# Kernel tuning notes

Measured on AMD Instinct MI355X. Metric: run time of the kernel, lower is better.

## Reference

```python
import jax, jax.numpy as jnp
import numpy as np

NUM_INSTANCES = 200
H = W = 128
PIXEL_EMB = 16   # input channels to the conditional conv
CHANNELS = 8     # num_init_channels (cond-inst hidden channels)
DEPTH = 3        # parsed from network_type 'cond_inst3'
# num_params = (16*8+8) + (8*8+8) + (8*1+1) = 217
NUM_PARAMS = (PIXEL_EMB * CHANNELS + CHANNELS) + (CHANNELS * CHANNELS + CHANNELS) + (CHANNELS + 1)


def setup_inputs() -> dict:
    key = jax.random.key(0)
    k1, k2 = jax.random.split(key)
    instance_embedding = jax.random.normal(k1, (NUM_INSTANCES, NUM_PARAMS), dtype=jnp.float32)
    pixel_embedding = jax.random.normal(k2, (NUM_INSTANCES, H, W, PIXEL_EMB), dtype=jnp.float32)
    return {"instance_embedding": instance_embedding,
            "pixel_embedding": pixel_embedding,
            "training": False}


def _per_pixel_conditional_conv(x, params, channels, depth):
    """x: [N,H,W,Cin], params: [N,P]. Chained per-instance 1x1 dynamic convs."""
    in_ch = x.shape[-1]
    start = 0
    out = x
    for i in range(depth):
        ch = 1 if i == depth - 1 else channels
        n = in_ch * ch + ch
        p = params[:, start:start + n]
        start += n
        w = p[:, :in_ch * ch].reshape(-1, in_ch, ch)   # [N, Cin, Cout]
        b = p[:, in_ch * ch:]                          # [N, Cout]
        out = jnp.einsum('nhwc,nck->nhwk', out, w) + b[:, None, None, :]
        if i != depth - 1:
            out = jax.nn.relu(out)
        in_ch = ch
    return out  # [N,H,W,1]


def reference(instance_embedding, pixel_embedding, training):
    # network_type='cond_inst3': backbone and project_out are identities;
    # instance params drive a depth-3 per-pixel conditional conv.
    out = _per_pixel_conditional_conv(pixel_embedding, instance_embedding,
                                      CHANNELS, DEPTH)
    return jnp.squeeze(out, axis=-1)  # [N,H,W]
```

## Files before the change

kernel.cpp:

```cpp
#include <hip/hip_runtime.h>


constexpr int NI = 200;
constexpr int HW = 128 * 128;
constexpr int PE = 16;
constexpr int CH = 8;
constexpr int NP = PE * CH + CH + (CH * CH + CH) + (CH + 1);

constexpr int THREADS = 256;
constexpr int PPT = 4;
constexpr int PIX_PER_BLOCK = THREADS * PPT;
constexpr int BLOCKS_PER_INST = HW / PIX_PER_BLOCK;

constexpr int OFF_W0 = 0;
constexpr int OFF_B0 = 128;
constexpr int OFF_W1 = 136;
constexpr int OFF_B1 = 200;
constexpr int OFF_W2 = 208;
constexpr int OFF_B2 = 216;

__global__ __launch_bounds__(THREADS) void maskhead_kernel(
    const float* __restrict__ inst,
    const float* __restrict__ pix,
    float* __restrict__ out)
{
    __shared__ float sp[NP];
    const int n = blockIdx.x / BLOCKS_PER_INST;
    const int chunk = blockIdx.x % BLOCKS_PER_INST;
    const int t = threadIdx.x;

    if (t < NP) sp[t] = inst[n * NP + t];
    __syncthreads();

    const size_t pixBase = (size_t)n * HW + (size_t)chunk * PIX_PER_BLOCK;

    float x[PPT][PE];
#pragma unroll
    for (int p = 0; p < PPT; ++p) {
        const float4* src =
            reinterpret_cast<const float4*>(pix + (pixBase + (size_t)p * THREADS + t) * PE);
#pragma unroll
        for (int q = 0; q < 4; ++q) {
            float4 v = src[q];
            x[p][q * 4 + 0] = v.x;
            x[p][q * 4 + 1] = v.y;
            x[p][q * 4 + 2] = v.z;
            x[p][q * 4 + 3] = v.w;
        }
    }

    float a[PPT][CH];
    {
        float4 blo = *reinterpret_cast<const float4*>(&sp[OFF_B0]);
        float4 bhi = *reinterpret_cast<const float4*>(&sp[OFF_B0 + 4]);
#pragma unroll
        for (int p = 0; p < PPT; ++p) {
            a[p][0] = blo.x; a[p][1] = blo.y; a[p][2] = blo.z; a[p][3] = blo.w;
            a[p][4] = bhi.x; a[p][5] = bhi.y; a[p][6] = bhi.z; a[p][7] = bhi.w;
        }
#pragma unroll
        for (int c = 0; c < PE; ++c) {
            float4 wlo = *reinterpret_cast<const float4*>(&sp[OFF_W0 + c * CH]);
            float4 whi = *reinterpret_cast<const float4*>(&sp[OFF_W0 + c * CH + 4]);
#pragma unroll
            for (int p = 0; p < PPT; ++p) {
                const float xv = x[p][c];
                a[p][0] = fmaf(xv, wlo.x, a[p][0]);
                a[p][1] = fmaf(xv, wlo.y, a[p][1]);
                a[p][2] = fmaf(xv, wlo.z, a[p][2]);
                a[p][3] = fmaf(xv, wlo.w, a[p][3]);
                a[p][4] = fmaf(xv, whi.x, a[p][4]);
                a[p][5] = fmaf(xv, whi.y, a[p][5]);
                a[p][6] = fmaf(xv, whi.z, a[p][6]);
                a[p][7] = fmaf(xv, whi.w, a[p][7]);
            }
        }
#pragma unroll
        for (int p = 0; p < PPT; ++p)
#pragma unroll
            for (int k = 0; k < CH; ++k) a[p][k] = fmaxf(a[p][k], 0.0f);
    }

    float y[PPT][CH];
    {
        float4 blo = *reinterpret_cast<const float4*>(&sp[OFF_B1]);
        float4 bhi = *reinterpret_cast<const float4*>(&sp[OFF_B1 + 4]);
#pragma unroll
        for (int p = 0; p < PPT; ++p) {
            y[p][0] = blo.x; y[p][1] = blo.y; y[p][2] = blo.z; y[p][3] = blo.w;
            y[p][4] = bhi.x; y[p][5] = bhi.y; y[p][6] = bhi.z; y[p][7] = bhi.w;
        }
#pragma unroll
        for (int c = 0; c < CH; ++c) {
            float4 wlo = *reinterpret_cast<const float4*>(&sp[OFF_W1 + c * CH]);
            float4 whi = *reinterpret_cast<const float4*>(&sp[OFF_W1 + c * CH + 4]);
#pragma unroll
            for (int p = 0; p < PPT; ++p) {
                const float xv = a[p][c];
                y[p][0] = fmaf(xv, wlo.x, y[p][0]);
                y[p][1] = fmaf(xv, wlo.y, y[p][1]);
                y[p][2] = fmaf(xv, wlo.z, y[p][2]);
                y[p][3] = fmaf(xv, wlo.w, y[p][3]);
                y[p][4] = fmaf(xv, whi.x, y[p][4]);
                y[p][5] = fmaf(xv, whi.y, y[p][5]);
                y[p][6] = fmaf(xv, whi.z, y[p][6]);
                y[p][7] = fmaf(xv, whi.w, y[p][7]);
            }
        }
#pragma unroll
        for (int p = 0; p < PPT; ++p)
#pragma unroll
            for (int k = 0; k < CH; ++k) y[p][k] = fmaxf(y[p][k], 0.0f);
    }

    {
        float4 wlo = *reinterpret_cast<const float4*>(&sp[OFF_W2]);
        float4 whi = *reinterpret_cast<const float4*>(&sp[OFF_W2 + 4]);
        const float b2 = sp[OFF_B2];
#pragma unroll
        for (int p = 0; p < PPT; ++p) {
            float o = b2;
            o = fmaf(y[p][0], wlo.x, o);
            o = fmaf(y[p][1], wlo.y, o);
            o = fmaf(y[p][2], wlo.z, o);
            o = fmaf(y[p][3], wlo.w, o);
            o = fmaf(y[p][4], whi.x, o);
            o = fmaf(y[p][5], whi.y, o);
            o = fmaf(y[p][6], whi.z, o);
            o = fmaf(y[p][7], whi.w, o);
            out[pixBase + (size_t)p * THREADS + t] = o;
        }
    }
}

extern "C" void kernel_launch(void* const* d_in, const int* in_sizes, int n_in,
                              void* d_out, int out_size, void* d_ws, size_t ws_size,
                              hipStream_t stream) {
    const float* inst = (const float*)d_in[0];
    const float* pix  = (const float*)d_in[1];
    float* out        = (float*)d_out;

    const int grid = NI * BLOCKS_PER_INST;
    maskhead_kernel<<<grid, THREADS, 0, stream>>>(inst, pix, out);
}
```

Measured before the change: 295.1 us.

## Split each pixel across four lanes for coalesced loads and shuffle reductions

Each pixel's 16 input channels are now spread over 4 lanes of a wave, one float4 each. Adjacent lanes therefore read contiguous memory, replacing the old pattern where each thread read 64 strided bytes per pixel. Partial sums for the first layer are combined with xor-shuffles. The second and final layers are split so each lane computes two hidden channels, and shuffles reduce the final output. Each block now covers 256 pixels instead of 1024, so the grid grows fourfold and there are extra cross-lane shuffle operations.

```diff
diff --git a/kernel.cpp b/kernel.cpp
--- a/kernel.cpp
+++ b/kernel.cpp
@@ -8,8 +8,8 @@
 constexpr int NP = PE * CH + CH + (CH * CH + CH) + (CH + 1);
 
 constexpr int THREADS = 256;
-constexpr int PPT = 4;
-constexpr int PIX_PER_BLOCK = THREADS * PPT;
+constexpr int PIX_PER_WAVE = 64;
+constexpr int PIX_PER_BLOCK = (THREADS / 64) * PIX_PER_WAVE;
 constexpr int BLOCKS_PER_INST = HW / PIX_PER_BLOCK;
 
 constexpr int OFF_W0 = 0;
@@ -32,105 +32,82 @@
     if (t < NP) sp[t] = inst[n * NP + t];
     __syncthreads();
 
-    const size_t pixBase = (size_t)n * HW + (size_t)chunk * PIX_PER_BLOCK;
+    const int lane = t & 63;
+    const int wave = t >> 6;
+    const int j = lane & 3;
+    const int g = lane >> 2;
 
-    float x[PPT][PE];
+    float w0s[4][CH];
 #pragma unroll
-    for (int p = 0; p < PPT; ++p) {
-        const float4* src =
-            reinterpret_cast<const float4*>(pix + (pixBase + (size_t)p * THREADS + t) * PE);
+    for (int c = 0; c < 4; ++c) {
+        float4 lo = *reinterpret_cast<const float4*>(&sp[OFF_W0 + (4 * j + c) * CH]);
+        float4 hi = *reinterpret_cast<const float4*>(&sp[OFF_W0 + (4 * j + c) * CH + 4]);
+        w0s[c][0] = lo.x; w0s[c][1] = lo.y; w0s[c][2] = lo.z; w0s[c][3] = lo.w;
+        w0s[c][4] = hi.x; w0s[c][5] = hi.y; w0s[c][6] = hi.z; w0s[c][7] = hi.w;
+    }
+    float b0s[CH];
+    {
+        float4 lo = *reinterpret_cast<const float4*>(&sp[OFF_B0]);
+        float4 hi = *reinterpret_cast<const float4*>(&sp[OFF_B0 + 4]);
+        b0s[0] = lo.x; b0s[1] = lo.y; b0s[2] = lo.z; b0s[3] = lo.w;
+        b0s[4] = hi.x; b0s[5] = hi.y; b0s[6] = hi.z; b0s[7] = hi.w;
+    }
+    float w1s[CH][2];
 #pragma unroll
-        for (int q = 0; q < 4; ++q) {
-            float4 v = src[q];
-            x[p][q * 4 + 0] = v.x;
-            x[p][q * 4 + 1] = v.y;
-            x[p][q * 4 + 2] = v.z;
-            x[p][q * 4 + 3] = v.w;
+    for (int m = 0; m < CH; ++m) {
+        w1s[m][0] = sp[OFF_W1 + m * CH + 2 * j];
+        w1s[m][1] = sp[OFF_W1 + m * CH + 2 * j + 1];
+    }
+    const float b1s0 = sp[OFF_B1 + 2 * j];
+    const float b1s1 = sp[OFF_B1 + 2 * j + 1];
+    const float w2s0 = sp[OFF_W2 + 2 * j];
+    const float w2s1 = sp[OFF_W2 + 2 * j + 1];
+    const float b2   = sp[OFF_B2];
+
+    const size_t pixBase = (size_t)n * HW + (size_t)chunk * PIX_PER_BLOCK
+                         + (size_t)wave * PIX_PER_WAVE;
+    const float4* src = reinterpret_cast<const float4*>(pix) + pixBase * 4 + lane;
+
+    float r[4];
+#pragma unroll
+    for (int k = 0; k < 4; ++k) {
+        const float4 v = src[k * 64];
+        const float xx[4] = {v.x, v.y, v.z, v.w};
+
+        float acc[CH];
+#pragma unroll
+        for (int q = 0; q < CH; ++q) acc[q] = 0.0f;
+#pragma unroll
+        for (int c = 0; c < 4; ++c)
+#pragma unroll
+            for (int q = 0; q < CH; ++q)
+                acc[q] = fmaf(xx[c], w0s[c][q], acc[q]);
+
+#pragma unroll
+        for (int q = 0; q < CH; ++q) acc[q] += __shfl_xor(acc[q], 1);
+#pragma unroll
+        for (int q = 0; q < CH; ++q) acc[q] += __shfl_xor(acc[q], 2);
+
+#pragma unroll
+        for (int q = 0; q < CH; ++q) acc[q] = fmaxf(acc[q] + b0s[q], 0.0f);
+
+        float y0 = b1s0, y1 = b1s1;
+#pragma unroll
+        for (int m = 0; m < CH; ++m) {
+            y0 = fmaf(acc[m], w1s[m][0], y0);
+            y1 = fmaf(acc[m], w1s[m][1], y1);
         }
+        y0 = fmaxf(y0, 0.0f);
+        y1 = fmaxf(y1, 0.0f);
+
+        float o = fmaf(y1, w2s1, y0 * w2s0);
+        o += __shfl_xor(o, 1);
+        o += __shfl_xor(o, 2);
+        r[k] = o + b2;
     }
 
-    float a[PPT][CH];
-    {
-        float4 blo = *reinterpret_cast<const float4*>(&sp[OFF_B0]);
-        float4 bhi = *reinterpret_cast<const float4*>(&sp[OFF_B0 + 4]);
-#pragma unroll
-        for (int p = 0; p < PPT; ++p) {
-            a[p][0] = blo.x; a[p][1] = blo.y; a[p][2] = blo.z; a[p][3] = blo.w;
-            a[p][4] = bhi.x; a[p][5] = bhi.y; a[p][6] = bhi.z; a[p][7] = bhi.w;
-        }
-#pragma unroll
-        for (int c = 0; c < PE; ++c) {
-            float4 wlo = *reinterpret_cast<const float4*>(&sp[OFF_W0 + c * CH]);
-            float4 whi = *reinterpret_cast<const float4*>(&sp[OFF_W0 + c * CH + 4]);
-#pragma unroll
-            for (int p = 0; p < PPT; ++p) {
-                const float xv = x[p][c];
-                a[p][0] = fmaf(xv, wlo.x, a[p][0]);
-                a[p][1] = fmaf(xv, wlo.y, a[p][1]);
-                a[p][2] = fmaf(xv, wlo.z, a[p][2]);
-                a[p][3] = fmaf(xv, wlo.w, a[p][3]);
-                a[p][4] = fmaf(xv, whi.x, a[p][4]);
-                a[p][5] = fmaf(xv, whi.y, a[p][5]);
-                a[p][6] = fmaf(xv, whi.z, a[p][6]);
-                a[p][7] = fmaf(xv, whi.w, a[p][7]);
-            }
-        }
-#pragma unroll
-        for (int p = 0; p < PPT; ++p)
-#pragma unroll
-            for (int k = 0; k < CH; ++k) a[p][k] = fmaxf(a[p][k], 0.0f);
-    }
-
-    float y[PPT][CH];
-    {
-        float4 blo = *reinterpret_cast<const float4*>(&sp[OFF_B1]);
-        float4 bhi = *reinterpret_cast<const float4*>(&sp[OFF_B1 + 4]);
-#pragma unroll
-        for (int p = 0; p < PPT; ++p) {
-            y[p][0] = blo.x; y[p][1] = blo.y; y[p][2] = blo.z; y[p][3] = blo.w;
-            y[p][4] = bhi.x; y[p][5] = bhi.y; y[p][6] = bhi.z; y[p][7] = bhi.w;
-        }
-#pragma unroll
-        for (int c = 0; c < CH; ++c) {
-            float4 wlo = *reinterpret_cast<const float4*>(&sp[OFF_W1 + c * CH]);
-            float4 whi = *reinterpret_cast<const float4*>(&sp[OFF_W1 + c * CH + 4]);
-#pragma unroll
-            for (int p = 0; p < PPT; ++p) {
-                const float xv = a[p][c];
-                y[p][0] = fmaf(xv, wlo.x, y[p][0]);
-                y[p][1] = fmaf(xv, wlo.y, y[p][1]);
-                y[p][2] = fmaf(xv, wlo.z, y[p][2]);
-                y[p][3] = fmaf(xv, wlo.w, y[p][3]);
-                y[p][4] = fmaf(xv, whi.x, y[p][4]);
-                y[p][5] = fmaf(xv, whi.y, y[p][5]);
-                y[p][6] = fmaf(xv, whi.z, y[p][6]);
-                y[p][7] = fmaf(xv, whi.w, y[p][7]);
-            }
-        }
-#pragma unroll
-        for (int p = 0; p < PPT; ++p)
-#pragma unroll
-            for (int k = 0; k < CH; ++k) y[p][k] = fmaxf(y[p][k], 0.0f);
-    }
-
-    {
-        float4 wlo = *reinterpret_cast<const float4*>(&sp[OFF_W2]);
-        float4 whi = *reinterpret_cast<const float4*>(&sp[OFF_W2 + 4]);
-        const float b2 = sp[OFF_B2];
-#pragma unroll
-        for (int p = 0; p < PPT; ++p) {
-            float o = b2;
-            o = fmaf(y[p][0], wlo.x, o);
-            o = fmaf(y[p][1], wlo.y, o);
-            o = fmaf(y[p][2], wlo.z, o);
-            o = fmaf(y[p][3], wlo.w, o);
-            o = fmaf(y[p][4], whi.x, o);
-            o = fmaf(y[p][5], whi.y, o);
-            o = fmaf(y[p][6], whi.z, o);
-            o = fmaf(y[p][7], whi.w, o);
-            out[pixBase + (size_t)p * THREADS + t] = o;
-        }
-    }
+    const float oval = (j == 0) ? r[0] : (j == 1) ? r[1] : (j == 2) ? r[2] : r[3];
+    out[pixBase + (size_t)(j * 16 + g)] = oval;
 }
 
 extern "C" void kernel_launch(void* const* d_in, const int* in_sizes, int n_in,
```

Result: faster. 288.6 us (-2.2%).
